# Kernel tuning notes

Measured on AMD Instinct MI355X. Metric: run time of the kernel, lower is better.

The kernel has to match this reference:

```python
import jax, jax.numpy as jnp
import numpy as np

N_NODES = 50000
N_EDGES = 800000
F_IN = 24
H = 128
N_GRAPHS = 100
BN_EPS = 1e-5


def setup_inputs() -> dict:
    key = jax.random.key(0)
    ks = jax.random.split(key, 12)
    x = jax.random.normal(ks[0], (N_NODES, F_IN), dtype=jnp.float32)
    edge_index = jax.random.randint(ks[1], (2, N_EDGES), 0, N_NODES, dtype=jnp.int32)
    batch = (jnp.arange(N_NODES, dtype=jnp.int32) // (N_NODES // N_GRAPHS)).astype(jnp.int32)

    def lin(k, fan_in, fan_out):
        bound = 1.0 / np.sqrt(fan_in)
        kw, kb = jax.random.split(k)
        W = jax.random.uniform(kw, (fan_in, fan_out), jnp.float32, -bound, bound)
        b = jax.random.uniform(kb, (fan_out,), jnp.float32, -bound, bound)
        return W, b

    W1, b1 = lin(ks[2], 2 * F_IN, H)
    W2, b2 = lin(ks[3], 2 * H, H)
    W3, b3 = lin(ks[4], 2 * H, H)
    Wl, bl = lin(ks[5], H, 1)
    g1 = jnp.ones((H,), jnp.float32); be1 = jnp.zeros((H,), jnp.float32)
    g2 = jnp.ones((H,), jnp.float32); be2 = jnp.zeros((H,), jnp.float32)
    g3 = jnp.ones((H,), jnp.float32); be3 = jnp.zeros((H,), jnp.float32)
    return {"x": x, "edge_index": edge_index, "batch": batch,
            "W1": W1, "b1": b1, "W2": W2, "b2": b2, "W3": W3, "b3": b3,
            "g1": g1, "be1": be1, "g2": g2, "be2": be2, "g3": g3, "be3": be3,
            "Wl": Wl, "bl": bl}


def edge_conv(x, src, dst, W, b):
    # PyG EdgeConv: message = mlp([x_i, x_j - x_i]) for edge j->i, aggr=max at i
    x_i = x[dst]                                    # [E, F]
    e = jnp.concatenate([x_i, x[src] - x_i], axis=-1)  # [E, 2F]
    m = jax.nn.relu(e @ W + b)                      # [E, H]
    out = jax.ops.segment_max(m, dst, num_segments=N_NODES)
    return jnp.where(jnp.isfinite(out), out, 0.0)   # isolated nodes -> 0


def batch_norm(h, g, b):
    # training-mode BN over node dim (biased variance), dropout treated as identity
    mu = h.mean(axis=0)
    var = ((h - mu) ** 2).mean(axis=0)
    return g * (h - mu) * jax.lax.rsqrt(var + BN_EPS) + b


def reference(x, edge_index, batch, W1, b1, W2, b2, W3, b3,
              g1, be1, g2, be2, g3, be3, Wl, bl):
    src, dst = edge_index[0], edge_index[1]
    h = edge_conv(x, src, dst, W1, b1)
    h = jax.nn.relu(batch_norm(h, g1, be1))
    h = edge_conv(h, src, dst, W2, b2)
    h = jax.nn.relu(batch_norm(h, g2, be2))
    h = edge_conv(h, src, dst, W3, b3)
    h = batch_norm(h, g3, be3)
    # global_mean_pool
    sums = jax.ops.segment_sum(h, batch, num_segments=N_GRAPHS)           # [G, H]
    counts = jax.ops.segment_sum(jnp.ones((h.shape[0],), h.dtype), batch,
                                 num_segments=N_GRAPHS)
    pooled = sums / jnp.maximum(counts, 1.0)[:, None]
    return jax.nn.relu(pooled @ Wl + bl)                                  # [G, 1]
```

## Files before the change

kernel.cpp:

```cpp
#include <hip/hip_runtime.h>

#define N_NODES 50000
#define N_EDGES 800000
#define F_IN 24
#define HDIM 128
#define N_GRAPHS 100
#define BN_EPS 1e-5f
#define NBLK 196
#define ROWS_PER_GRAPH (N_NODES / N_GRAPHS)
#define MM_GRID 782
#define HIST_BLKS ((N_EDGES + 255) / 256)
#define PREP_BLKS (F_IN + 2 * HDIM)
#define SSTR 32
#define SUMS_PER_LAYER (256 * SSTR)
#define STATS_BLKS 392
#define POOL_CHUNKS 10
#define POOL_BLKS (N_GRAPHS * POOL_CHUNKS)
#define ROWS_PER_CHUNK (ROWS_PER_GRAPH / POOL_CHUNKS)


typedef _Float16 h2 __attribute__((ext_vector_type(2)));
typedef _Float16 h4 __attribute__((ext_vector_type(4)));
typedef _Float16 f16x8 __attribute__((ext_vector_type(8)));
typedef float f32x4 __attribute__((ext_vector_type(4)));

__device__ inline h4 max4(h4 a, h4 b) { return __builtin_elementwise_max(a, b); }
__device__ inline h4 shfl_xor_h4(h4 v, int m) {
    union { h4 h; int2 i; } u;
    u.h = v;
    u.i.x = __shfl_xor(u.i.x, m);
    u.i.y = __shfl_xor(u.i.y, m);
    return u.h;
}

template <int K, int KC>
__global__ __launch_bounds__(256) void k_mm1(const float* __restrict__ X,
                                             const float* __restrict__ Wcat,
                                             const float* __restrict__ bias,
                                             _Float16* __restrict__ A, _Float16* __restrict__ C,
                                             const int* __restrict__ src,
                                             const int* __restrict__ dst,
                                             const unsigned* __restrict__ off,
                                             const unsigned* __restrict__ rank,
                                             unsigned* __restrict__ ssrc) {
    __shared__ float Xs[KC * 68];
    __shared__ float Ws[KC * 256];
    if (blockIdx.x >= MM_GRID) {
        int e = (blockIdx.x - MM_GRID) * 256 + threadIdx.x;
        if (e < N_EDGES)
            ssrc[off[dst[e]] + rank[e]] = (unsigned)src[e];
        return;
    }
    int tid = threadIdx.x;
    int row0 = blockIdx.x * 64;
    int cg = tid & 31;
    int rg = tid >> 5;

    float accA[8][4], accC[8][4];
#pragma unroll
    for (int ri = 0; ri < 8; ++ri)
#pragma unroll
        for (int ci = 0; ci < 4; ++ci) {
            accA[ri][ci] = bias[cg * 4 + ci];
            accC[ri][ci] = 0.f;
        }

    for (int k0 = 0; k0 < K; k0 += KC) {
        __syncthreads();
        {
            const int C4 = KC / 4;
            for (int i = tid; i < 64 * C4; i += 256) {
                int c4 = i % C4, r = i / C4;
                int row = row0 + r;
                float4 v = make_float4(0.f, 0.f, 0.f, 0.f);
                if (row < N_NODES) v = *(const float4*)&X[row * K + k0 + c4 * 4];
                Xs[(c4 * 4 + 0) * 68 + r] = v.x;
                Xs[(c4 * 4 + 1) * 68 + r] = v.y;
                Xs[(c4 * 4 + 2) * 68 + r] = v.z;
                Xs[(c4 * 4 + 3) * 68 + r] = v.w;
            }
        }
        for (int i = tid; i < KC * 64; i += 256) {
            int c4 = i & 63, kr = i >> 6;
            *(float4*)&Ws[kr * 256 + c4 * 4] =
                *(const float4*)&Wcat[(k0 + kr) * 256 + c4 * 4];
        }
        __syncthreads();
#pragma unroll
        for (int kk = 0; kk < KC; ++kk) {
            float4 t0 = *(const float4*)&Xs[kk * 68 + rg * 8];
            float4 t1 = *(const float4*)&Xs[kk * 68 + rg * 8 + 4];
            float4 wa = *(const float4*)&Ws[kk * 256 + cg * 4];
            float4 wc = *(const float4*)&Ws[kk * 256 + 128 + cg * 4];
            float t[8] = {t0.x, t0.y, t0.z, t0.w, t1.x, t1.y, t1.z, t1.w};
            float wav[4] = {wa.x, wa.y, wa.z, wa.w};
            float wcv[4] = {wc.x, wc.y, wc.z, wc.w};
#pragma unroll
            for (int ri = 0; ri < 8; ++ri)
#pragma unroll
                for (int ci = 0; ci < 4; ++ci) {
                    accA[ri][ci] += t[ri] * wav[ci];
                    accC[ri][ci] += t[ri] * wcv[ci];
                }
        }
    }

#pragma unroll
    for (int ri = 0; ri < 8; ++ri) {
        int row = row0 + rg * 8 + ri;
        if (row < N_NODES) {
            union { h2 h[2]; uint2 u; } pa;
            pa.h[0] = h2{(_Float16)accA[ri][0], (_Float16)accA[ri][1]};
            pa.h[1] = h2{(_Float16)accA[ri][2], (_Float16)accA[ri][3]};
            *(uint2*)&A[row * HDIM + cg * 4] = pa.u;
            union { h2 h[2]; uint2 u; } pk;
            pk.h[0] = h2{(_Float16)accC[ri][0], (_Float16)accC[ri][1]};
            pk.h[1] = h2{(_Float16)accC[ri][2], (_Float16)accC[ri][3]};
            *(uint2*)&C[row * HDIM + cg * 4] = pk.u;
        }
    }
}

__global__ __launch_bounds__(256) void k_mmf(const _Float16* __restrict__ X,
                                             const _Float16* __restrict__ Wf,
                                             const float* __restrict__ bias,
                                             const float* __restrict__ sums,
                                             const float* __restrict__ g,
                                             const float* __restrict__ be,
                                             _Float16* __restrict__ A, _Float16* __restrict__ C) {
    __shared__ _Float16 Xh[16 * 520];
    __shared__ _Float16 Wh[128 * 128];
    __shared__ float scs[128], shs[128];
    int tid = threadIdx.x;
    int lane = tid & 63, wv = tid >> 6;
    int row0 = blockIdx.x * 64;

    if (tid < 128) {
        float S  = sums[tid * SSTR];
        float S2 = sums[(128 + tid) * SSTR];
        float mean = S / (float)N_NODES;
        float var = fmaxf(S2 / (float)N_NODES - mean * mean, 0.f);
        float scv = g[tid] / sqrtf(var + BN_EPS);
        scs[tid] = scv;
        shs[tid] = be[tid] - mean * scv;
    }
    {
        const uint4* s = (const uint4*)Wf;
        uint4* d = (uint4*)Wh;
        for (int i = tid; i < 2048; i += 256) d[i] = s[i];
    }
    __syncthreads();
    for (int i = tid; i < 64 * 32; i += 256) {
        int k4 = i & 31, rl = i >> 5;
        int row = row0 + rl;
        float4 v = make_float4(0.f, 0.f, 0.f, 0.f);
        if (row < N_NODES) {
            h4 xv = *(const h4*)&X[row * HDIM + k4 * 4];
            v = make_float4((float)xv.x, (float)xv.y, (float)xv.z, (float)xv.w);
        }
        int c = k4 * 4;
        v.x = fmaxf(v.x * scs[c + 0] + shs[c + 0], 0.f);
        v.y = fmaxf(v.y * scs[c + 1] + shs[c + 1], 0.f);
        v.z = fmaxf(v.z * scs[c + 2] + shs[c + 2], 0.f);
        v.w = fmaxf(v.w * scs[c + 3] + shs[c + 3], 0.f);
        int rt = rl >> 4, m = rl & 15, kc = k4 >> 3, q = (k4 >> 1) & 3, jh = k4 & 1;
        _Float16* dp = Xh + (rt * 4 + kc) * 520 + (q * 16 + m) * 8 + jh * 4;
        dp[0] = (_Float16)v.x; dp[1] = (_Float16)v.y;
        dp[2] = (_Float16)v.z; dp[3] = (_Float16)v.w;
    }
    __syncthreads();

    int n = lane & 15, q = lane >> 4;
    f32x4 acc[8];

#pragma unroll
    for (int nt = 0; nt < 8; ++nt) {
        float b0 = bias[nt * 16 + n];
        acc[nt] = f32x4{b0, b0, b0, b0};
    }
#pragma unroll
    for (int kc = 0; kc < 4; ++kc) {
        f16x8 a = *(const f16x8*)(Xh + (wv * 4 + kc) * 520 + lane * 8);
#pragma unroll
        for (int nt = 0; nt < 8; ++nt) {
            f16x8 b = *(const f16x8*)(Wh + ((nt * 4 + kc) * 64 + lane) * 8);
            acc[nt] = __builtin_amdgcn_mfma_f32_16x16x32_f16(a, b, acc[nt], 0, 0, 0);
        }
    }
#pragma unroll
    for (int nt = 0; nt < 8; ++nt) {
#pragma unroll
        for (int r = 0; r < 4; ++r) {
            int row = row0 + wv * 16 + q * 4 + r;
            if (row < N_NODES) A[row * HDIM + nt * 16 + n] = (_Float16)acc[nt][r];
        }
    }
    __syncthreads();
    {
        const uint4* s = (const uint4*)(Wf + 16384);
        uint4* d = (uint4*)Wh;
        for (int i = tid; i < 2048; i += 256) d[i] = s[i];
    }
    __syncthreads();

#pragma unroll
    for (int nt = 0; nt < 8; ++nt) acc[nt] = f32x4{0.f, 0.f, 0.f, 0.f};
#pragma unroll
    for (int kc = 0; kc < 4; ++kc) {
        f16x8 a = *(const f16x8*)(Xh + (wv * 4 + kc) * 520 + lane * 8);
#pragma unroll
        for (int nt = 0; nt < 8; ++nt) {
            f16x8 b = *(const f16x8*)(Wh + ((nt * 4 + kc) * 64 + lane) * 8);
            acc[nt] = __builtin_amdgcn_mfma_f32_16x16x32_f16(a, b, acc[nt], 0, 0, 0);
        }
    }
#pragma unroll
    for (int nt = 0; nt < 8; ++nt) {
#pragma unroll
        for (int r = 0; r < 4; ++r) {
            int row = row0 + wv * 16 + q * 4 + r;
            if (row < N_NODES) C[row * HDIM + nt * 16 + n] = (_Float16)acc[nt][r];
        }
    }
}

__global__ void k_pre(const float* __restrict__ W1, const float* __restrict__ W2,
                      const float* __restrict__ W3, float* __restrict__ Wcat1,
                      _Float16* __restrict__ Wf2, _Float16* __restrict__ Wf3,
                      const int* __restrict__ dst, unsigned* __restrict__ deg,
                      unsigned* __restrict__ rank) {
    int b = blockIdx.x;
    int j = threadIdx.x;
    if (b < F_IN) {
        float wb = W1[(b + F_IN) * HDIM + (j & 127)];
        float wt = W1[b * HDIM + (j & 127)];
        Wcat1[b * 256 + j] = (j < HDIM) ? (wt - wb) : wb;
    } else if (b < PREP_BLKS) {
        int idx = b - F_IN;
        int layer = idx >> 7;
        int k = idx & 127;
        const float* W = layer ? W3 : W2;
        _Float16* Wf   = layer ? Wf3 : Wf2;
        int col = j & 127;
        float wt = W[k * HDIM + col];
        float wb = W[(k + HDIM) * HDIM + col];
        float v = (j < 128) ? (wt - wb) : wb;
        int plane = j >> 7;
        int nt = col >> 4, n = col & 15, kc = k >> 5, q = (k >> 3) & 3, jj = k & 7;
        int f = ((nt * 4 + kc) * 4 + q) * 128 + n * 8 + jj;
        Wf[plane * 16384 + f] = (_Float16)v;
    } else {
        int e = (b - PREP_BLKS) * 256 + j;
        if (e < N_EDGES) rank[e] = atomicAdd(&deg[dst[e]], 1u);
    }
}

__global__ __launch_bounds__(256) void k_scanall(const unsigned* __restrict__ deg,
                                                 unsigned* __restrict__ bsum,
                                                 unsigned* __restrict__ off) {
    __shared__ unsigned s[256];
    int t = threadIdx.x;
    int b = blockIdx.x;
    int i = b * 256 + t;
    unsigned v = (i < N_NODES) ? deg[i] : 0u;
    s[t] = v;
    __syncthreads();
    for (int d = 1; d < 256; d <<= 1) {
        unsigned u = (t >= d) ? s[t - d] : 0u;
        __syncthreads();
        s[t] += u;
        __syncthreads();
    }
    unsigned locex = s[t] - v;
    if (t == 255) atomicExch(&bsum[b], s[255] + 1u);
    __syncthreads();
    unsigned bs = 0;
    if (t < NBLK) {
        unsigned x;
        do { x = atomicAdd(&bsum[t], 0u); } while (x == 0u);
        bs = x - 1u;
    }
    s[t] = (t < NBLK) ? bs : 0u;
    __syncthreads();
    for (int d = 1; d < 256; d <<= 1) {
        unsigned u = (t >= d) ? s[t - d] : 0u;
        __syncthreads();
        s[t] += u;
        __syncthreads();
    }
    unsigned bexcl = (b == 0) ? 0u : s[b - 1];
    if (i < N_NODES) off[i] = bexcl + locex;
}

__global__ __launch_bounds__(256) void k_agg(const h4* __restrict__ A,
                                             const h4* __restrict__ Cc,
                                             const unsigned* __restrict__ off,
                                             const unsigned* __restrict__ deg,
                                             const unsigned* __restrict__ ssrc,
                                             h4* __restrict__ H) {
    __shared__ unsigned sl[4][64];
    int w = threadIdx.x >> 6;
    int lane = threadIdx.x & 63;
    int i = blockIdx.x * 4 + w;
    int d = (int)deg[i];
    unsigned o = off[i];
    int half = lane >> 5;
    int cl = lane & 31;
    h4 a = A[i * 32 + cl];
    union { unsigned short us[4]; h4 v; } nif;
    nif.us[0] = 0xFC00; nif.us[1] = 0xFC00; nif.us[2] = 0xFC00; nif.us[3] = 0xFC00;
    const h4 NI = nif.v;
    h4 m = NI;
    for (int base = 0; base < d; base += 64) {
        int cnt = min(64, d - base);
        if (lane < cnt) sl[w][lane] = ssrc[o + base + lane];
        int e = 0;
        for (; e + 16 <= cnt; e += 16) {
            unsigned s[8];
#pragma unroll
            for (int j = 0; j < 8; ++j) s[j] = sl[w][e + 2 * j + half];
            h4 v[8];
#pragma unroll
            for (int j = 0; j < 8; ++j) v[j] = Cc[s[j] * 32 + cl];
#pragma unroll
            for (int st = 4; st > 0; st >>= 1)
#pragma unroll
                for (int j = 0; j < st; ++j) v[j] = max4(v[j], v[j + st]);
            m = max4(m, v[0]);
        }
        if (e < cnt) {
            int last = cnt - 1;
            unsigned s[8];
#pragma unroll
            for (int j = 0; j < 8; ++j) {
                int idx = e + 2 * j + half;
                s[j] = sl[w][idx < last ? idx : last];
            }
            h4 v[8];
#pragma unroll
            for (int j = 0; j < 8; ++j) v[j] = Cc[s[j] * 32 + cl];
#pragma unroll
            for (int j = 0; j < 8; ++j) {
                int idx = e + 2 * j + half;
                if (idx >= cnt) v[j] = NI;
            }
#pragma unroll
            for (int st = 4; st > 0; st >>= 1)
#pragma unroll
                for (int j = 0; j < st; ++j) v[j] = max4(v[j], v[j + st]);
            m = max4(m, v[0]);
        }
    }
    m = max4(m, shfl_xor_h4(m, 32));
    if (lane < 32) {
        float h0 = (d > 0) ? fmaxf((float)a.x + (float)m.x, 0.f) : 0.f;
        float h1 = (d > 0) ? fmaxf((float)a.y + (float)m.y, 0.f) : 0.f;
        float h2v = (d > 0) ? fmaxf((float)a.z + (float)m.z, 0.f) : 0.f;
        float h3 = (d > 0) ? fmaxf((float)a.w + (float)m.w, 0.f) : 0.f;
        H[i * 32 + cl] = h4{(_Float16)h0, (_Float16)h1, (_Float16)h2v, (_Float16)h3};
    }
}

__global__ __launch_bounds__(256) void k_stats(const _Float16* __restrict__ H,
                                               float* __restrict__ sums) {
    __shared__ float4 ls[256], ls2[256];
    int t = threadIdx.x;
    int c4 = t & 31, rg = t >> 5;
    int row0 = blockIdx.x * 128;
    float4 s = make_float4(0.f, 0.f, 0.f, 0.f);
    float4 s2 = make_float4(0.f, 0.f, 0.f, 0.f);
#pragma unroll 4
    for (int it = 0; it < 16; ++it) {
        int row = row0 + rg * 16 + it;
        if (row < N_NODES) {
            h4 hv = *(const h4*)&H[row * HDIM + c4 * 4];
            float4 v = make_float4((float)hv.x, (float)hv.y, (float)hv.z, (float)hv.w);
            s.x += v.x; s.y += v.y; s.z += v.z; s.w += v.w;
            s2.x += v.x * v.x; s2.y += v.y * v.y; s2.z += v.z * v.z; s2.w += v.w * v.w;
        }
    }
    ls[t] = s; ls2[t] = s2;
    __syncthreads();
    if (t < 32) {
        float4 a = ls[t], a2 = ls2[t];
#pragma unroll
        for (int j = 1; j < 8; ++j) {
            float4 b = ls[j * 32 + t], b2 = ls2[j * 32 + t];
            a.x += b.x; a.y += b.y; a.z += b.z; a.w += b.w;
            a2.x += b2.x; a2.y += b2.y; a2.z += b2.z; a2.w += b2.w;
        }
        int c = t * 4;
        atomicAdd(&sums[(c + 0) * SSTR], a.x);
        atomicAdd(&sums[(c + 1) * SSTR], a.y);
        atomicAdd(&sums[(c + 2) * SSTR], a.z);
        atomicAdd(&sums[(c + 3) * SSTR], a.w);
        atomicAdd(&sums[(128 + c + 0) * SSTR], a2.x);
        atomicAdd(&sums[(128 + c + 1) * SSTR], a2.y);
        atomicAdd(&sums[(128 + c + 2) * SSTR], a2.z);
        atomicAdd(&sums[(128 + c + 3) * SSTR], a2.w);
    }
}

__global__ __launch_bounds__(256) void k_pool2(const _Float16* __restrict__ H,
                                               float* __restrict__ Pp,
                                               float* __restrict__ sums) {
    __shared__ float4 ls[256], ls2[256];
    int t = threadIdx.x;
    int c4 = t & 31, rg = t >> 5;
    int b = blockIdx.x;
    int base = (b / POOL_CHUNKS) * ROWS_PER_GRAPH + (b % POOL_CHUNKS) * ROWS_PER_CHUNK;
    float4 s = make_float4(0.f, 0.f, 0.f, 0.f);
    float4 s2 = make_float4(0.f, 0.f, 0.f, 0.f);
#pragma unroll
    for (int j = 0; j < 7; ++j) {
        int rl = rg + j * 8;
        if (rl < ROWS_PER_CHUNK) {
            int row = base + rl;
            h4 hv = *(const h4*)&H[row * HDIM + c4 * 4];
            float4 v = make_float4((float)hv.x, (float)hv.y, (float)hv.z, (float)hv.w);
            s.x += v.x; s.y += v.y; s.z += v.z; s.w += v.w;
            s2.x += v.x * v.x; s2.y += v.y * v.y; s2.z += v.z * v.z; s2.w += v.w * v.w;
        }
    }
    ls[t] = s; ls2[t] = s2;
    __syncthreads();
    if (t < 32) {
        float4 a = ls[t], a2 = ls2[t];
#pragma unroll
        for (int j = 1; j < 8; ++j) {
            float4 q = ls[j * 32 + t], q2 = ls2[j * 32 + t];
            a.x += q.x; a.y += q.y; a.z += q.z; a.w += q.w;
            a2.x += q2.x; a2.y += q2.y; a2.z += q2.z; a2.w += q2.w;
        }
        int c = t * 4;
        *(float4*)&Pp[b * HDIM + c] = a;
        atomicAdd(&sums[(c + 0) * SSTR], a.x);
        atomicAdd(&sums[(c + 1) * SSTR], a.y);
        atomicAdd(&sums[(c + 2) * SSTR], a.z);
        atomicAdd(&sums[(c + 3) * SSTR], a.w);
        atomicAdd(&sums[(128 + c + 0) * SSTR], a2.x);
        atomicAdd(&sums[(128 + c + 1) * SSTR], a2.y);
        atomicAdd(&sums[(128 + c + 2) * SSTR], a2.z);
        atomicAdd(&sums[(128 + c + 3) * SSTR], a2.w);
    }
}

__global__ __launch_bounds__(128) void k_out(const float* __restrict__ Pp,
                                             const float* __restrict__ sums,
                                             const float* __restrict__ g3,
                                             const float* __restrict__ be3,
                                             const float* __restrict__ Wl,
                                             const float* __restrict__ bl,
                                             float* __restrict__ out) {
    int g = blockIdx.x;
    int k = threadIdx.x;
    float S  = sums[k * SSTR];
    float S2 = sums[(128 + k) * SSTR];
    float mean = S / (float)N_NODES;
    float var = fmaxf(S2 / (float)N_NODES - mean * mean, 0.f);
    float scv = g3[k] / sqrtf(var + BN_EPS);
    float shv = be3[k] - mean * scv;
    float pooled = 0.f;
#pragma unroll
    for (int j = 0; j < POOL_CHUNKS; ++j)
        pooled += Pp[(g * POOL_CHUNKS + j) * HDIM + k];
    float p = (scv * (pooled * (1.f / (float)ROWS_PER_GRAPH)) + shv) * Wl[k];
    __shared__ float red[2];
    for (int o = 32; o > 0; o >>= 1) p += __shfl_down(p, o);
    if ((k & 63) == 0) red[k >> 6] = p;
    __syncthreads();
    if (k == 0) out[g] = fmaxf(red[0] + red[1] + bl[0], 0.f);
}

extern "C" void kernel_launch(void* const* d_in, const int* in_sizes, int n_in,
                              void* d_out, int out_size, void* d_ws, size_t ws_size,
                              hipStream_t stream) {
    const float* x   = (const float*)d_in[0];
    const int* ei    = (const int*)d_in[1];
    const float* W1  = (const float*)d_in[3];
    const float* b1  = (const float*)d_in[4];
    const float* W2  = (const float*)d_in[5];
    const float* b2  = (const float*)d_in[6];
    const float* W3  = (const float*)d_in[7];
    const float* b3  = (const float*)d_in[8];
    const float* g1  = (const float*)d_in[9];
    const float* be1 = (const float*)d_in[10];
    const float* g2  = (const float*)d_in[11];
    const float* be2 = (const float*)d_in[12];
    const float* g3  = (const float*)d_in[13];
    const float* be3 = (const float*)d_in[14];
    const float* Wl  = (const float*)d_in[15];
    const float* bl  = (const float*)d_in[16];
    float* out = (float*)d_out;

    const int* srcp = ei;
    const int* dstp = ei + N_EDGES;

    char* ws = (char*)d_ws;
    size_t o = 0;
    auto alloc = [&](size_t bytes) -> void* {
        o = (o + 255) & ~(size_t)255;
        void* p = ws + o;
        o += bytes;
        return p;
    };
    _Float16* A   = (_Float16*)alloc((size_t)N_NODES * HDIM * 2);
    _Float16* C   = (_Float16*)alloc((size_t)N_NODES * HDIM * 2);
    _Float16* h   = (_Float16*)alloc((size_t)N_NODES * HDIM * 2);
    float* Wcat1  = (float*)alloc((size_t)F_IN * 256 * 4);
    _Float16* Wf2 = (_Float16*)alloc((size_t)2 * 16384 * 2);
    _Float16* Wf3 = (_Float16*)alloc((size_t)2 * 16384 * 2);
    unsigned* deg  = (unsigned*)alloc((size_t)N_NODES * 4);
    unsigned* bsum = (unsigned*)alloc((size_t)NBLK * 4);
    float* sums    = (float*)alloc((size_t)3 * SUMS_PER_LAYER * 4);
    unsigned* off  = (unsigned*)alloc((size_t)N_NODES * 4);
    unsigned* rank = (unsigned*)alloc((size_t)N_EDGES * 4);
    unsigned* ssrc = (unsigned*)alloc((size_t)N_EDGES * 4);
    float* Pp      = (float*)alloc((size_t)POOL_BLKS * HDIM * 4);
    (void)ws_size; (void)n_in; (void)in_sizes; (void)out_size;

    float* sums0 = sums;
    float* sums1 = sums + SUMS_PER_LAYER;
    float* sums2 = sums + 2 * SUMS_PER_LAYER;

    size_t zlen = (size_t)((char*)(sums + 3 * SUMS_PER_LAYER) - (char*)deg);
    (void)hipMemsetAsync(deg, 0, zlen, stream);

    k_pre<<<PREP_BLKS + HIST_BLKS, 256, 0, stream>>>(W1, W2, W3, Wcat1, Wf2, Wf3,
                                                     dstp, deg, rank);
    k_scanall<<<NBLK, 256, 0, stream>>>(deg, bsum, off);

    const int AGB = N_NODES / 4;

    k_mm1<F_IN, F_IN><<<MM_GRID + HIST_BLKS, 256, 0, stream>>>(
        x, Wcat1, b1, A, C, srcp, dstp, off, rank, ssrc);
    k_agg<<<AGB, 256, 0, stream>>>((const h4*)A, (const h4*)C, off, deg, ssrc, (h4*)h);
    k_stats<<<STATS_BLKS, 256, 0, stream>>>(h, sums0);

    k_mmf<<<MM_GRID, 256, 0, stream>>>(h, Wf2, b2, sums0, g1, be1, A, C);
    k_agg<<<AGB, 256, 0, stream>>>((const h4*)A, (const h4*)C, off, deg, ssrc, (h4*)h);
    k_stats<<<STATS_BLKS, 256, 0, stream>>>(h, sums1);

    k_mmf<<<MM_GRID, 256, 0, stream>>>(h, Wf3, b3, sums1, g2, be2, A, C);
    k_agg<<<AGB, 256, 0, stream>>>((const h4*)A, (const h4*)C, off, deg, ssrc, (h4*)h);

    k_pool2<<<POOL_BLKS, 256, 0, stream>>>(h, Pp, sums2);
    k_out<<<N_GRAPHS, 128, 0, stream>>>(Pp, sums2, g3, be3, Wl, bl, out);
}
```

Measured before the change: 355.3 us.

## Fuse stats, scan+scatter, and pool+out kernels via in-kernel grid barriers

```diff
diff --git a/kernel.cpp b/kernel.cpp
--- a/kernel.cpp
+++ b/kernel.cpp
@@ -13,7 +13,7 @@
 #define PREP_BLKS (F_IN + 2 * HDIM)
 #define SSTR 32
 #define SUMS_PER_LAYER (256 * SSTR)
-#define STATS_BLKS 392
+#define STATS_TILES 392
 #define POOL_CHUNKS 10
 #define POOL_BLKS (N_GRAPHS * POOL_CHUNKS)
 #define ROWS_PER_CHUNK (ROWS_PER_GRAPH / POOL_CHUNKS)
@@ -37,20 +37,9 @@
 __global__ __launch_bounds__(256) void k_mm1(const float* __restrict__ X,
                                              const float* __restrict__ Wcat,
                                              const float* __restrict__ bias,
-                                             _Float16* __restrict__ A, _Float16* __restrict__ C,
-                                             const int* __restrict__ src,
-                                             const int* __restrict__ dst,
-                                             const unsigned* __restrict__ off,
-                                             const unsigned* __restrict__ rank,
-                                             unsigned* __restrict__ ssrc) {
+                                             _Float16* __restrict__ A, _Float16* __restrict__ C) {
     __shared__ float Xs[KC * 68];
     __shared__ float Ws[KC * 256];
-    if (blockIdx.x >= MM_GRID) {
-        int e = (blockIdx.x - MM_GRID) * 256 + threadIdx.x;
-        if (e < N_EDGES)
-            ssrc[off[dst[e]] + rank[e]] = (unsigned)src[e];
-        return;
-    }
     int tid = threadIdx.x;
     int row0 = blockIdx.x * 64;
     int cg = tid & 31;
@@ -124,16 +113,69 @@
 __global__ __launch_bounds__(256) void k_mmf(const _Float16* __restrict__ X,
                                              const _Float16* __restrict__ Wf,
                                              const float* __restrict__ bias,
-                                             const float* __restrict__ sums,
+                                             float* __restrict__ sums,
                                              const float* __restrict__ g,
                                              const float* __restrict__ be,
-                                             _Float16* __restrict__ A, _Float16* __restrict__ C) {
+                                             _Float16* __restrict__ A, _Float16* __restrict__ C,
+                                             unsigned* __restrict__ ticket,
+                                             unsigned* __restrict__ done) {
     __shared__ _Float16 Xh[16 * 520];
-    __shared__ _Float16 Wh[128 * 128];
+    __shared__ __attribute__((aligned(16))) _Float16 Wh[128 * 128];
     __shared__ float scs[128], shs[128];
+    __shared__ int tkt;
     int tid = threadIdx.x;
     int lane = tid & 63, wv = tid >> 6;
     int row0 = blockIdx.x * 64;
+
+    {
+        float4* ls  = (float4*)Wh;
+        float4* ls2 = ls + 256;
+        for (;;) {
+            if (tid == 0) tkt = (int)atomicAdd(ticket, 1u);
+            __syncthreads();
+            int b = tkt;
+            if (b >= STATS_TILES) break;
+            int c4 = tid & 31, rg = tid >> 5;
+            int r0 = b * 128;
+            float4 s = make_float4(0.f, 0.f, 0.f, 0.f);
+            float4 s2 = make_float4(0.f, 0.f, 0.f, 0.f);
+#pragma unroll 4
+            for (int it = 0; it < 16; ++it) {
+                int row = r0 + rg * 16 + it;
+                if (row < N_NODES) {
+                    h4 hv = *(const h4*)&X[row * HDIM + c4 * 4];
+                    float4 v = make_float4((float)hv.x, (float)hv.y, (float)hv.z, (float)hv.w);
+                    s.x += v.x; s.y += v.y; s.z += v.z; s.w += v.w;
+                    s2.x += v.x * v.x; s2.y += v.y * v.y; s2.z += v.z * v.z; s2.w += v.w * v.w;
+                }
+            }
+            ls[tid] = s; ls2[tid] = s2;
+            __syncthreads();
+            if (tid < 32) {
+                float4 a = ls[tid], a2 = ls2[tid];
+#pragma unroll
+                for (int j = 1; j < 8; ++j) {
+                    float4 bb = ls[j * 32 + tid], b2 = ls2[j * 32 + tid];
+                    a.x += bb.x; a.y += bb.y; a.z += bb.z; a.w += bb.w;
+                    a2.x += b2.x; a2.y += b2.y; a2.z += b2.z; a2.w += b2.w;
+                }
+                int c = tid * 4;
+                atomicAdd(&sums[(c + 0) * SSTR], a.x);
+                atomicAdd(&sums[(c + 1) * SSTR], a.y);
+                atomicAdd(&sums[(c + 2) * SSTR], a.z);
+                atomicAdd(&sums[(c + 3) * SSTR], a.w);
+                atomicAdd(&sums[(128 + c + 0) * SSTR], a2.x);
+                atomicAdd(&sums[(128 + c + 1) * SSTR], a2.y);
+                atomicAdd(&sums[(128 + c + 2) * SSTR], a2.z);
+                atomicAdd(&sums[(128 + c + 3) * SSTR], a2.w);
+            }
+            __syncthreads();
+            if (tid == 0) atomicAdd(done, 1u);
+            __syncthreads();
+        }
+        if (tid == 0) { while (atomicAdd(done, 0u) < STATS_TILES) {} }
+        __syncthreads();
+    }
 
     if (tid < 128) {
         float S  = sums[tid * SSTR];
@@ -255,41 +297,61 @@
     }
 }
 
-__global__ __launch_bounds__(256) void k_scanall(const unsigned* __restrict__ deg,
-                                                 unsigned* __restrict__ bsum,
-                                                 unsigned* __restrict__ off) {
+__global__ __launch_bounds__(256) void k_scansc(const unsigned* __restrict__ deg,
+                                                unsigned* __restrict__ bsum,
+                                                unsigned* __restrict__ off,
+                                                const int* __restrict__ src,
+                                                const int* __restrict__ dst,
+                                                const unsigned* __restrict__ rank,
+                                                unsigned* __restrict__ ssrc,
+                                                unsigned* __restrict__ ticket,
+                                                unsigned* __restrict__ done) {
     __shared__ unsigned s[256];
+    __shared__ int tkt;
     int t = threadIdx.x;
-    int b = blockIdx.x;
-    int i = b * 256 + t;
-    unsigned v = (i < N_NODES) ? deg[i] : 0u;
-    s[t] = v;
-    __syncthreads();
-    for (int d = 1; d < 256; d <<= 1) {
-        unsigned u = (t >= d) ? s[t - d] : 0u;
-        __syncthreads();
-        s[t] += u;
-        __syncthreads();
-    }
-    unsigned locex = s[t] - v;
-    if (t == 255) atomicExch(&bsum[b], s[255] + 1u);
-    __syncthreads();
-    unsigned bs = 0;
-    if (t < NBLK) {
-        unsigned x;
-        do { x = atomicAdd(&bsum[t], 0u); } while (x == 0u);
-        bs = x - 1u;
-    }
-    s[t] = (t < NBLK) ? bs : 0u;
-    __syncthreads();
-    for (int d = 1; d < 256; d <<= 1) {
-        unsigned u = (t >= d) ? s[t - d] : 0u;
-        __syncthreads();
-        s[t] += u;
-        __syncthreads();
-    }
-    unsigned bexcl = (b == 0) ? 0u : s[b - 1];
-    if (i < N_NODES) off[i] = bexcl + locex;
+    for (;;) {
+        if (t == 0) tkt = (int)atomicAdd(ticket, 1u);
+        __syncthreads();
+        int b = tkt;
+        if (b >= NBLK) break;
+        int i = b * 256 + t;
+        unsigned v = (i < N_NODES) ? deg[i] : 0u;
+        s[t] = v;
+        __syncthreads();
+        for (int d = 1; d < 256; d <<= 1) {
+            unsigned u = (t >= d) ? s[t - d] : 0u;
+            __syncthreads();
+            s[t] += u;
+            __syncthreads();
+        }
+        unsigned locex = s[t] - v;
+        if (t == 255) atomicExch(&bsum[b], s[255] + 1u);
+        __syncthreads();
+        unsigned bs = 0;
+        if (t < NBLK) {
+            unsigned x;
+            do { x = atomicAdd(&bsum[t], 0u); } while (x == 0u);
+            bs = x - 1u;
+        }
+        s[t] = (t < NBLK) ? bs : 0u;
+        __syncthreads();
+        for (int d = 1; d < 256; d <<= 1) {
+            unsigned u = (t >= d) ? s[t - d] : 0u;
+            __syncthreads();
+            s[t] += u;
+            __syncthreads();
+        }
+        unsigned bexcl = (b == 0) ? 0u : s[b - 1];
+        if (i < N_NODES) atomicExch(&off[i], bexcl + locex);
+        __syncthreads();
+        if (t == 0) atomicAdd(done, 1u);
+        __syncthreads();
+    }
+    if (t == 0) { while (atomicAdd(done, 0u) < NBLK) {} }
+    __syncthreads();
+    int e = blockIdx.x * 256 + t;
+    if (e < N_EDGES)
+        ssrc[off[dst[e]] + rank[e]] = (unsigned)src[e];
 }
 
 __global__ __launch_bounds__(256) void k_agg(const h4* __restrict__ A,
@@ -361,18 +423,28 @@
     }
 }
 
-__global__ __launch_bounds__(256) void k_stats(const _Float16* __restrict__ H,
-                                               float* __restrict__ sums) {
+__global__ __launch_bounds__(256) void k_poolout(const _Float16* __restrict__ H,
+                                                 float* __restrict__ Pp,
+                                                 float* __restrict__ sums,
+                                                 const float* __restrict__ g3,
+                                                 const float* __restrict__ be3,
+                                                 const float* __restrict__ Wl,
+                                                 const float* __restrict__ bl,
+                                                 float* __restrict__ out,
+                                                 unsigned* __restrict__ done) {
     __shared__ float4 ls[256], ls2[256];
+    __shared__ float red[2];
     int t = threadIdx.x;
     int c4 = t & 31, rg = t >> 5;
-    int row0 = blockIdx.x * 128;
+    int b = blockIdx.x;
+    int base = (b / POOL_CHUNKS) * ROWS_PER_GRAPH + (b % POOL_CHUNKS) * ROWS_PER_CHUNK;
     float4 s = make_float4(0.f, 0.f, 0.f, 0.f);
     float4 s2 = make_float4(0.f, 0.f, 0.f, 0.f);
-#pragma unroll 4
-    for (int it = 0; it < 16; ++it) {
-        int row = row0 + rg * 16 + it;
-        if (row < N_NODES) {
+#pragma unroll
+    for (int j = 0; j < 7; ++j) {
+        int rl = rg + j * 8;
+        if (rl < ROWS_PER_CHUNK) {
+            int row = base + rl;
             h4 hv = *(const h4*)&H[row * HDIM + c4 * 4];
             float4 v = make_float4((float)hv.x, (float)hv.y, (float)hv.z, (float)hv.w);
             s.x += v.x; s.y += v.y; s.z += v.z; s.w += v.w;
@@ -385,11 +457,15 @@
         float4 a = ls[t], a2 = ls2[t];
 #pragma unroll
         for (int j = 1; j < 8; ++j) {
-            float4 b = ls[j * 32 + t], b2 = ls2[j * 32 + t];
-            a.x += b.x; a.y += b.y; a.z += b.z; a.w += b.w;
-            a2.x += b2.x; a2.y += b2.y; a2.z += b2.z; a2.w += b2.w;
+            float4 q = ls[j * 32 + t], q2 = ls2[j * 32 + t];
+            a.x += q.x; a.y += q.y; a.z += q.z; a.w += q.w;
+            a2.x += q2.x; a2.y += q2.y; a2.z += q2.z; a2.w += q2.w;
         }
         int c = t * 4;
+        atomicExch((unsigned*)&Pp[b * HDIM + c + 0], __float_as_uint(a.x));
+        atomicExch((unsigned*)&Pp[b * HDIM + c + 1], __float_as_uint(a.y));
+        atomicExch((unsigned*)&Pp[b * HDIM + c + 2], __float_as_uint(a.z));
+        atomicExch((unsigned*)&Pp[b * HDIM + c + 3], __float_as_uint(a.w));
         atomicAdd(&sums[(c + 0) * SSTR], a.x);
         atomicAdd(&sums[(c + 1) * SSTR], a.y);
         atomicAdd(&sums[(c + 2) * SSTR], a.z);
@@ -399,77 +475,32 @@
         atomicAdd(&sums[(128 + c + 2) * SSTR], a2.z);
         atomicAdd(&sums[(128 + c + 3) * SSTR], a2.w);
     }
-}
-
-__global__ __launch_bounds__(256) void k_pool2(const _Float16* __restrict__ H,
-                                               float* __restrict__ Pp,
-                                               float* __restrict__ sums) {
-    __shared__ float4 ls[256], ls2[256];
-    int t = threadIdx.x;
-    int c4 = t & 31, rg = t >> 5;
-    int b = blockIdx.x;
-    int base = (b / POOL_CHUNKS) * ROWS_PER_GRAPH + (b % POOL_CHUNKS) * ROWS_PER_CHUNK;
-    float4 s = make_float4(0.f, 0.f, 0.f, 0.f);
-    float4 s2 = make_float4(0.f, 0.f, 0.f, 0.f);
-#pragma unroll
-    for (int j = 0; j < 7; ++j) {
-        int rl = rg + j * 8;
-        if (rl < ROWS_PER_CHUNK) {
-            int row = base + rl;
-            h4 hv = *(const h4*)&H[row * HDIM + c4 * 4];
-            float4 v = make_float4((float)hv.x, (float)hv.y, (float)hv.z, (float)hv.w);
-            s.x += v.x; s.y += v.y; s.z += v.z; s.w += v.w;
-            s2.x += v.x * v.x; s2.y += v.y * v.y; s2.z += v.z * v.z; s2.w += v.w * v.w;
-        }
-    }
-    ls[t] = s; ls2[t] = s2;
-    __syncthreads();
-    if (t < 32) {
-        float4 a = ls[t], a2 = ls2[t];
-#pragma unroll
-        for (int j = 1; j < 8; ++j) {
-            float4 q = ls[j * 32 + t], q2 = ls2[j * 32 + t];
-            a.x += q.x; a.y += q.y; a.z += q.z; a.w += q.w;
-            a2.x += q2.x; a2.y += q2.y; a2.z += q2.z; a2.w += q2.w;
-        }
-        int c = t * 4;
-        *(float4*)&Pp[b * HDIM + c] = a;
-        atomicAdd(&sums[(c + 0) * SSTR], a.x);
-        atomicAdd(&sums[(c + 1) * SSTR], a.y);
-        atomicAdd(&sums[(c + 2) * SSTR], a.z);
-        atomicAdd(&sums[(c + 3) * SSTR], a.w);
-        atomicAdd(&sums[(128 + c + 0) * SSTR], a2.x);
-        atomicAdd(&sums[(128 + c + 1) * SSTR], a2.y);
-        atomicAdd(&sums[(128 + c + 2) * SSTR], a2.z);
-        atomicAdd(&sums[(128 + c + 3) * SSTR], a2.w);
-    }
-}
-
-__global__ __launch_bounds__(128) void k_out(const float* __restrict__ Pp,
-                                             const float* __restrict__ sums,
-                                             const float* __restrict__ g3,
-                                             const float* __restrict__ be3,
-                                             const float* __restrict__ Wl,
-                                             const float* __restrict__ bl,
-                                             float* __restrict__ out) {
-    int g = blockIdx.x;
-    int k = threadIdx.x;
-    float S  = sums[k * SSTR];
-    float S2 = sums[(128 + k) * SSTR];
-    float mean = S / (float)N_NODES;
-    float var = fmaxf(S2 / (float)N_NODES - mean * mean, 0.f);
-    float scv = g3[k] / sqrtf(var + BN_EPS);
-    float shv = be3[k] - mean * scv;
-    float pooled = 0.f;
-#pragma unroll
-    for (int j = 0; j < POOL_CHUNKS; ++j)
-        pooled += Pp[(g * POOL_CHUNKS + j) * HDIM + k];
-    float p = (scv * (pooled * (1.f / (float)ROWS_PER_GRAPH)) + shv) * Wl[k];
-    __shared__ float red[2];
+    __syncthreads();
+    if (t == 0) atomicAdd(done, 1u);
+
+    if (b >= N_GRAPHS) return;
+    if (t == 0) { while (atomicAdd(done, 0u) < POOL_BLKS) {} }
+    __syncthreads();
+
+    int gidx = b;
+    float p = 0.f;
+    if (t < 128) {
+        float S  = sums[t * SSTR];
+        float S2 = sums[(128 + t) * SSTR];
+        float mean = S / (float)N_NODES;
+        float var = fmaxf(S2 / (float)N_NODES - mean * mean, 0.f);
+        float scv = g3[t] / sqrtf(var + BN_EPS);
+        float shv = be3[t] - mean * scv;
+        float pooled = 0.f;
+#pragma unroll
+        for (int j = 0; j < POOL_CHUNKS; ++j)
+            pooled += Pp[(gidx * POOL_CHUNKS + j) * HDIM + t];
+        p = (scv * (pooled * (1.f / (float)ROWS_PER_GRAPH)) + shv) * Wl[t];
+    }
     for (int o = 32; o > 0; o >>= 1) p += __shfl_down(p, o);
-    if ((k & 63) == 0) red[k >> 6] = p;
-    __syncthreads();
-    if (k == 0) out[g] = fmaxf(red[0] + red[1] + bl[0], 0.f);
+    if (t < 128 && (t & 63) == 0) red[t >> 6] = p;
+    __syncthreads();
+    if (t == 0) out[gidx] = fmaxf(red[0] + red[1] + bl[0], 0.f);
 }
 
 extern "C" void kernel_launch(void* const* d_in, const int* in_sizes, int n_in,
@@ -513,6 +544,7 @@
     unsigned* deg  = (unsigned*)alloc((size_t)N_NODES * 4);
     unsigned* bsum = (unsigned*)alloc((size_t)NBLK * 4);
     float* sums    = (float*)alloc((size_t)3 * SUMS_PER_LAYER * 4);
+    unsigned* cnt  = (unsigned*)alloc((size_t)16 * 4);
     unsigned* off  = (unsigned*)alloc((size_t)N_NODES * 4);
     unsigned* rank = (unsigned*)alloc((size_t)N_EDGES * 4);
     unsigned* ssrc = (unsigned*)alloc((size_t)N_EDGES * 4);
@@ -523,27 +555,27 @@
     float* sums1 = sums + SUMS_PER_LAYER;
     float* sums2 = sums + 2 * SUMS_PER_LAYER;
 
-    size_t zlen = (size_t)((char*)(sums + 3 * SUMS_PER_LAYER) - (char*)deg);
+    size_t zlen = (size_t)((char*)(cnt + 16) - (char*)deg);
     (void)hipMemsetAsync(deg, 0, zlen, stream);
 
     k_pre<<<PREP_BLKS + HIST_BLKS, 256, 0, stream>>>(W1, W2, W3, Wcat1, Wf2, Wf3,
                                                      dstp, deg, rank);
-    k_scanall<<<NBLK, 256, 0, stream>>>(deg, bsum, off);
+    k_scansc<<<HIST_BLKS, 256, 0, stream>>>(deg, bsum, off, srcp, dstp, rank,
+                                            ssrc, &cnt[7], &cnt[6]);
 
     const int AGB = N_NODES / 4;
 
-    k_mm1<F_IN, F_IN><<<MM_GRID + HIST_BLKS, 256, 0, stream>>>(
-        x, Wcat1, b1, A, C, srcp, dstp, off, rank, ssrc);
+    k_mm1<F_IN, F_IN><<<MM_GRID, 256, 0, stream>>>(x, Wcat1, b1, A, C);
     k_agg<<<AGB, 256, 0, stream>>>((const h4*)A, (const h4*)C, off, deg, ssrc, (h4*)h);
-    k_stats<<<STATS_BLKS, 256, 0, stream>>>(h, sums0);
-
-    k_mmf<<<MM_GRID, 256, 0, stream>>>(h, Wf2, b2, sums0, g1, be1, A, C);
+
+    k_mmf<<<MM_GRID, 256, 0, stream>>>(h, Wf2, b2, sums0, g1, be1, A, C,
+                                       &cnt[0], &cnt[1]);
     k_agg<<<AGB, 256, 0, stream>>>((const h4*)A, (const h4*)C, off, deg, ssrc, (h4*)h);
-    k_stats<<<STATS_BLKS, 256, 0, stream>>>(h, sums1);
-
-    k_mmf<<<MM_GRID, 256, 0, stream>>>(h, Wf3, b3, sums1, g2, be2, A, C);
+
+    k_mmf<<<MM_GRID, 256, 0, stream>>>(h, Wf3, b3, sums1, g2, be2, A, C,
+                                       &cnt[2], &cnt[3]);
     k_agg<<<AGB, 256, 0, stream>>>((const h4*)A, (const h4*)C, off, deg, ssrc, (h4*)h);
 
-    k_pool2<<<POOL_BLKS, 256, 0, stream>>>(h, Pp, sums2);
-    k_out<<<N_GRAPHS, 128, 0, stream>>>(Pp, sums2, g3, be3, Wl, bl, out);
-}
+    k_poolout<<<POOL_BLKS, 256, 0, stream>>>(h, Pp, sums2, g3, be3, Wl, bl, out,
+                                             &cnt[5]);
+}
```

Result: slower. 532.0 us (+49.7%).
